# Kernel optimization log

Measured on AMD Instinct MI355X. Metric: run time of the kernel, lower is better.

## Reference

```python
import jax, jax.numpy as jnp
import numpy as np

NS = 50000; ND = 50000; E = 600000
C = 64; A = 16; S = 64; H = 8; M = 192; DH = C // H
EPS = 1e-5


def _ln(x, w, b):
    # EquivariantLayerNormV2 restricted to 0e irreps == standard affine LayerNorm
    x = x - jnp.mean(x, axis=-1, keepdims=True)
    v = jnp.mean(x * x, axis=-1, keepdims=True)
    return x * jax.lax.rsqrt(v + EPS) * w + b


def _forward(src_f, dst_f, edge_attr, edge_scalars, edge_logits, edge_src, edge_dst,
             ln_src_w, ln_src_b, W_src, ln_dst_w, ln_dst_b, W_dst, b_dst,
             W_ea, W_dtp, W_r1, b_r1, W_r2, b_r2, alpha_vec,
             W_proj, b_proj, ln_post_w, ln_post_b, W_f1, b_f1, W_f2, b_f2):
    # prenorm + linear projections of src/dst node features
    ms = _ln(src_f, ln_src_w, ln_src_b) @ W_src                      # [NS, C]
    md = _ln(dst_f, ln_dst_w, ln_dst_b) @ W_dst + b_dst              # [ND, C]
    msg = ms[edge_src] + md[edge_dst]                                # [E, C] gather
    # radial MLP on edge scalars modulates the (scalar-irrep) tensor-product weights
    r = jax.nn.silu(edge_scalars @ W_r1 + b_r1)                      # [E, S]
    w_edge = r @ W_r2 + b_r2                                         # [E, 2C]
    ea = edge_attr @ W_ea                                            # [E, C]
    dtp = ((msg * ea) @ W_dtp) * w_edge                              # [E, 2C]
    alpha_feat = dtp[:, :C].reshape(E, H, DH)
    val = dtp[:, C:].reshape(E, H, DH)
    # per-head attention logits + optional precomputed edge logits
    logits = jnp.sum(jax.nn.leaky_relu(alpha_feat, 0.2) * alpha_vec, axis=-1)  # [E, H]
    logits = logits + edge_logits[:, None]
    # softmax over incoming edges of each dst node (segment softmax)
    m = jax.ops.segment_max(logits, edge_dst, num_segments=ND)
    a = jnp.exp(logits - m[edge_dst])
    z = jax.ops.segment_sum(a, edge_dst, num_segments=ND)
    attn = a / z[edge_dst]                                           # [E, H]
    out = jax.ops.segment_sum((val * attn[..., None]).reshape(E, C), edge_dst,
                              num_segments=ND)                       # [ND, C] scatter
    out = out @ W_proj + b_proj
    emb = out + dst_f                                                # skip_1 (irreps match -> identity)
    y = _ln(emb, ln_post_w, ln_post_b)                               # post_norm
    ffn = jax.nn.silu(y @ W_f1 + b_f1) @ W_f2 + b_f2                 # FFN with swish gate (0e)
    return ffn + emb                                                 # skip_2


def setup_inputs() -> dict:
    key = jax.random.key(0)
    ks = jax.random.split(key, 20)
    def n(k, shape, scale=1.0):
        return jax.random.normal(k, shape, dtype=jnp.float32) * scale
    return {
        "src_f": n(ks[0], (NS, C)),
        "dst_f": n(ks[1], (ND, C)),
        "edge_attr": n(ks[2], (E, A)),
        "edge_scalars": jax.random.uniform(ks[3], (E, S), dtype=jnp.float32),
        "edge_logits": n(ks[4], (E,)),
        "edge_src": jax.random.randint(ks[5], (E,), 0, NS),
        "edge_dst": jax.random.randint(ks[6], (E,), 0, ND),
        "ln_src_w": jnp.ones((C,), jnp.float32), "ln_src_b": jnp.zeros((C,), jnp.float32),
        "W_src": n(ks[7], (C, C), C ** -0.5),
        "ln_dst_w": jnp.ones((C,), jnp.float32), "ln_dst_b": jnp.zeros((C,), jnp.float32),
        "W_dst": n(ks[8], (C, C), C ** -0.5), "b_dst": jnp.zeros((C,), jnp.float32),
        "W_ea": n(ks[9], (A, C), A ** -0.5),
        "W_dtp": n(ks[10], (C, 2 * C), C ** -0.5),
        "W_r1": n(ks[11], (S, S), S ** -0.5), "b_r1": jnp.zeros((S,), jnp.float32),
        "W_r2": n(ks[12], (S, 2 * C), S ** -0.5), "b_r2": jnp.zeros((2 * C,), jnp.float32),
        "alpha_vec": n(ks[13], (H, DH), DH ** -0.5),
        "W_proj": n(ks[14], (C, C), C ** -0.5), "b_proj": jnp.zeros((C,), jnp.float32),
        "ln_post_w": jnp.ones((C,), jnp.float32), "ln_post_b": jnp.zeros((C,), jnp.float32),
        "W_f1": n(ks[15], (C, M), C ** -0.5), "b_f1": jnp.zeros((M,), jnp.float32),
        "W_f2": n(ks[16], (M, C), M ** -0.5), "b_f2": jnp.zeros((C,), jnp.float32),
    }


def reference(src_f, dst_f, edge_attr, edge_scalars, edge_logits, edge_src, edge_dst,
              ln_src_w, ln_src_b, W_src, ln_dst_w, ln_dst_b, W_dst, b_dst,
              W_ea, W_dtp, W_r1, b_r1, W_r2, b_r2, alpha_vec,
              W_proj, b_proj, ln_post_w, ln_post_b, W_f1, b_f1, W_f2, b_f2):
    return _forward(src_f, dst_f, edge_attr, edge_scalars, edge_logits, edge_src, edge_dst,
                    ln_src_w, ln_src_b, W_src, ln_dst_w, ln_dst_b, W_dst, b_dst,
                    W_ea, W_dtp, W_r1, b_r1, W_r2, b_r2, alpha_vec,
                    W_proj, b_proj, ln_post_w, ln_post_b, W_f1, b_f1, W_f2, b_f2)
```

## Files before the change

### kernel.cpp

```cpp
#include <hip/hip_runtime.h>
#include <hip/hip_bf16.h>

typedef __hip_bfloat16 bf16;
typedef unsigned short u16;
typedef unsigned int u32;

#define NS_N 50000
#define ND_N 50000
#define NE_E 600000
#define C 64
#define AD 16
#define SD 64
#define NH 8
#define MF 192
#define EPSV 1e-5f

#define WB() __builtin_amdgcn_wave_barrier()

typedef short short8 __attribute__((ext_vector_type(8)));
typedef float f32x4 __attribute__((ext_vector_type(4)));
#define MFMA16(a, b, c) __builtin_amdgcn_mfma_f32_16x16x32_bf16(a, b, c, 0, 0, 0)

__device__ __forceinline__ float lo16(u32 u) {
    union { u32 i; float f; } v; v.i = u << 16; return v.f;
}
__device__ __forceinline__ float hi16(u32 u) {
    union { u32 i; float f; } v; v.i = u & 0xffff0000u; return v.f;
}
__device__ __forceinline__ float b2fu(u16 u) {
    union { u32 i; float f; } v; v.i = ((u32)u) << 16; return v.f;
}
__device__ __forceinline__ u16 f2bbits(float f) {
    u32 u = __float_as_uint(f);
    u32 r = u + 0x7FFFu + ((u >> 16) & 1u);
    return (u16)(r >> 16);
}
__device__ __forceinline__ float loadf(const void* p, size_t i, int isbf) {
    if (isbf) { union { u32 u; float f; } v; v.u = ((u32)((const u16*)p)[i]) << 16; return v.f; }
    return ((const float*)p)[i];
}
__device__ __forceinline__ u16 loadb(const void* p, size_t i, int isbf) {
    if (isbf) return ((const u16*)p)[i];
    return f2bbits(((const float*)p)[i]);
}
__device__ __forceinline__ short8 load8bf(const void* p, size_t off, int isbf) {
    if (isbf) return *(const short8*)((const u16*)p + off);
    const float4* q = (const float4*)((const float*)p + off);
    float4 f0 = q[0], f1 = q[1];
    short8 r;
    r[0] = (short)f2bbits(f0.x); r[1] = (short)f2bbits(f0.y);
    r[2] = (short)f2bbits(f0.z); r[3] = (short)f2bbits(f0.w);
    r[4] = (short)f2bbits(f1.x); r[5] = (short)f2bbits(f1.y);
    r[6] = (short)f2bbits(f1.z); r[7] = (short)f2bbits(f1.w);
    return r;
}

__device__ __forceinline__ float waveAllSum(float v) {
    #pragma unroll
    for (int off = 32; off >= 1; off >>= 1) v += __shfl_xor(v, off, 64);
    return v;
}

__global__ void detect_kernel(const void* src, int* flag) {
    const u16* p = (const u16*)src;
    const int lane = threadIdx.x;
    int cnt = 0;
    #pragma unroll
    for (int j = 0; j < 32; ++j) {
        u16 w = p[(size_t)(lane * 32 + j) * 2];
        int e = (w >> 7) & 0xFF;
        if (w == 0 || (e >= 100 && e <= 150)) cnt++;
    }
    #pragma unroll
    for (int off = 32; off >= 1; off >>= 1) cnt += __shfl_xor(cnt, off, 64);
    if (lane == 0) *flag = (cnt > 1536) ? 1 : 0;
}

__global__ void zero_int_kernel(int* p, int n) {
    int i = blockIdx.x * blockDim.x + threadIdx.x;
    if (i < n) p[i] = 0;
}

__global__ void hist_kernel(const int* __restrict__ edge_dst, int* __restrict__ cnt) {
    int e = blockIdx.x * blockDim.x + threadIdx.x;
    if (e < NE_E) atomicAdd(&cnt[edge_dst[e]], 1);
}

#define SCAN_CHUNK 1024
#define SCAN_NCH ((ND_N + SCAN_CHUNK - 1) / SCAN_CHUNK)

__global__ void scan_phase1(const int* __restrict__ cnt, int* __restrict__ chunksum) {
    __shared__ int wsum[4];
    const int b = blockIdx.x, tidx = threadIdx.x;
    const int base = b * SCAN_CHUNK + tidx * 4;
    int s = 0;
    if (base + 3 < ND_N) {
        int4 v = *(const int4*)&cnt[base];
        s = v.x + v.y + v.z + v.w;
    } else {
        #pragma unroll
        for (int j = 0; j < 4; ++j) { int i = base + j; if (i < ND_N) s += cnt[i]; }
    }
    #pragma unroll
    for (int off = 32; off >= 1; off >>= 1) s += __shfl_xor(s, off, 64);
    const int wv = tidx >> 6, lane = tidx & 63;
    if (lane == 0) wsum[wv] = s;
    __syncthreads();
    if (tidx == 0) chunksum[b] = wsum[0] + wsum[1] + wsum[2] + wsum[3];
}

__global__ void scan_phase3(const int* __restrict__ cnt, const int* __restrict__ chunksum,
                            int* __restrict__ row_ptr, int* __restrict__ cursor,
                            int* __restrict__ row_ptr_last) {
    __shared__ int woff[4];
    __shared__ int choff_s;
    const int b = blockIdx.x, tidx = threadIdx.x;
    if (tidx < 64) {
        int v = (tidx < SCAN_NCH) ? chunksum[tidx] : 0;
        int incl = v;
        #pragma unroll
        for (int off = 1; off < 64; off <<= 1) {
            int t = __shfl_up(incl, off, 64);
            if (tidx >= off) incl += t;
        }
        if (tidx == b) choff_s = incl - v;
        if (b == 0 && tidx == 63) *row_ptr_last = incl;
    }
    const int base = b * SCAN_CHUNK + tidx * 4;
    int v[4];
    #pragma unroll
    for (int j = 0; j < 4; ++j) { int i = base + j; v[j] = (i < ND_N) ? cnt[i] : 0; }
    int s = v[0] + v[1] + v[2] + v[3];
    int incl = s;
    const int lane = tidx & 63, wv = tidx >> 6;
    #pragma unroll
    for (int off = 1; off < 64; off <<= 1) {
        int t = __shfl_up(incl, off, 64);
        if (lane >= off) incl += t;
    }
    if (lane == 63) woff[wv] = incl;
    __syncthreads();
    int cross = 0;
    for (int w = 0; w < wv; ++w) cross += woff[w];
    int run = choff_s + cross + (incl - s);
    #pragma unroll
    for (int j = 0; j < 4; ++j) {
        int i = base + j;
        if (i < ND_N) { row_ptr[i] = run; cursor[i] = run; }
        run += v[j];
    }
}

__global__ void scatter_kernel(const int* __restrict__ edge_dst, int* __restrict__ cursor,
                               int* __restrict__ perm) {
    int e = blockIdx.x * blockDim.x + threadIdx.x;
    if (e < NE_E) {
        int pos = atomicAdd(&cursor[edge_dst[e]], 1);
        perm[pos] = e;
    }
}

__global__ void node_proj_kernel(const void* __restrict__ xf,
                                 const void* __restrict__ lnw, const void* __restrict__ lnb,
                                 const void* __restrict__ W, const void* __restrict__ bias,
                                 int has_bias, const int* __restrict__ flagp,
                                 float* __restrict__ out, int N) {
    __shared__ u16 sW[C * C];
    __shared__ float slnw[C], slnb[C], sbias[C];
    __shared__ float ybuf[4][C];

    const int isbf = *flagp;
    const int tid = threadIdx.x;
    for (int i = tid; i < C * C; i += blockDim.x) {
        int k = i >> 6, c = i & 63;
        sW[((k >> 1) << 7) + (c << 1) + (k & 1)] = loadb(W, i, isbf);
    }
    if (tid < C) {
        slnw[tid] = loadf(lnw, tid, isbf);
        slnb[tid] = loadf(lnb, tid, isbf);
        sbias[tid] = has_bias ? loadf(bias, tid, isbf) : 0.f;
    }
    __syncthreads();

    const int wave = tid >> 6, lane = tid & 63;
    const u32* w = (const u32*)sW;
    const int gw = blockIdx.x * 4 + wave, nw = gridDim.x * 4;
    for (int n = gw; n < N; n += nw) {
        float x = loadf(xf, (size_t)n * C + lane, isbf);
        float mean = waveAllSum(x) * (1.f / 64.f);
        float xc = x - mean;
        float var = waveAllSum(xc * xc) * (1.f / 64.f);
        float y = xc * rsqrtf(var + EPSV) * slnw[lane] + slnb[lane];
        WB();
        ybuf[wave][lane] = y;
        WB();
        float acc = sbias[lane];
        #pragma unroll 8
        for (int k2 = 0; k2 < 32; ++k2) {
            float2 yv = *(const float2*)&ybuf[wave][k2 * 2];
            u32 wp = w[(k2 << 6) + lane];
            acc += yv.x * lo16(wp) + yv.y * hi16(wp);
        }
        WB();
        out[(size_t)n * C + lane] = acc;
    }
}

__launch_bounds__(512, 4)
__global__ void edge_mfma_kernel(const void* __restrict__ edge_attr,
                                 const void* __restrict__ edge_scalars,
                                 const void* __restrict__ edge_logits,
                                 const int* __restrict__ edge_src,
                                 const int* __restrict__ edge_dst,
                                 const int* __restrict__ perm,
                                 const void* __restrict__ W_ea, const void* __restrict__ W_dtp,
                                 const void* __restrict__ W_r1, const void* __restrict__ b_r1,
                                 const void* __restrict__ W_r2, const void* __restrict__ b_r2,
                                 const void* __restrict__ alpha_vec,
                                 const int* __restrict__ flagp,
                                 const float* __restrict__ ms, const float* __restrict__ md,
                                 u16* __restrict__ valbuf, float* __restrict__ logitsbuf) {
    __shared__ u16 sWr1T[C * SD];
    __shared__ u16 sWr2T[2 * C * SD];
    __shared__ u16 sWdtpT[2 * C * C];
    __shared__ u16 sWeaT[C * 32];
    __shared__ float sbr1[SD], sbr2[2 * C], salpha[C];
    __shared__ u16 scratch[8][2][16 * C];

    const int isbf = *flagp;
    const int tid = threadIdx.x;
    for (int i = tid; i < SD * SD; i += 512) {
        int k = i >> 6, n = i & 63;
        sWr1T[n * 64 + (((k >> 3) ^ (n & 7)) << 3) + (k & 7)] = loadb(W_r1, i, isbf);
    }
    for (int i = tid; i < SD * 2 * C; i += 512) {
        int k = i >> 7, n = i & 127;
        sWr2T[n * 64 + (((k >> 3) ^ (n & 7)) << 3) + (k & 7)] = loadb(W_r2, i, isbf);
    }
    for (int i = tid; i < C * 2 * C; i += 512) {
        int k = i >> 7, n = i & 127;
        sWdtpT[n * 64 + (((k >> 3) ^ (n & 7)) << 3) + (k & 7)] = loadb(W_dtp, i, isbf);
    }
    for (int i = tid; i < C * 32; i += 512) {
        int n = i >> 5, k = i & 31;
        sWeaT[i] = (k < AD) ? loadb(W_ea, (size_t)k * C + n, isbf) : (u16)0;
    }
    for (int i = tid; i < SD; i += 512) sbr1[i] = loadf(b_r1, i, isbf);
    for (int i = tid; i < 2 * C; i += 512) sbr2[i] = loadf(b_r2, i, isbf);
    for (int i = tid; i < C; i += 512) salpha[i] = loadf(alpha_vec, i, isbf);
    __syncthreads();

    const int wv = tid >> 6, lane = tid & 63;
    const int m15 = lane & 15, quad = lane >> 4;
    const int sw = m15 & 7;
    const int pg0 = (quad ^ sw) << 3;
    const int pg1 = pg0 ^ 32;
    u16* scr_r = scratch[wv][0];
    u16* scr_e = scratch[wv][1];

    for (int t = blockIdx.x * 8 + wv; t < NE_E / 16; t += gridDim.x * 8) {
        const int e0 = t * 16;
        const int e = perm[e0 + m15];
        short8 esA0 = load8bf(edge_scalars, (size_t)e * SD + quad * 8, isbf);
        short8 esA1 = load8bf(edge_scalars, (size_t)e * SD + 32 + quad * 8, isbf);
        float elg_lane = loadf(edge_logits, e, isbf);
        WB();
        #pragma unroll
        for (int nt = 0; nt < 4; ++nt) {
            f32x4 c = {0.f, 0.f, 0.f, 0.f};
            c = MFMA16(esA0, *(const short8*)&sWr1T[(nt * 16 + m15) * 64 + pg0], c);
            c = MFMA16(esA1, *(const short8*)&sWr1T[(nt * 16 + m15) * 64 + pg1], c);
            float bc = sbr1[nt * 16 + m15];
            int lg = nt * 2 + (m15 >> 3);
            int o = m15 & 7;
            #pragma unroll
            for (int r = 0; r < 4; ++r) {
                float f = c[r] + bc;
                f = f / (1.f + __expf(-f));
                int row = quad * 4 + r;
                scr_r[row * 64 + ((lg ^ (row & 7)) << 3) + o] = f2bbits(f);
            }
        }
        short8 eaA = 0;
        if (quad < 2) eaA = load8bf(edge_attr, (size_t)e * AD + quad * 8, isbf);
        #pragma unroll
        for (int nt = 0; nt < 4; ++nt) {
            f32x4 c = {0.f, 0.f, 0.f, 0.f};
            c = MFMA16(eaA, *(const short8*)&sWeaT[(nt * 16 + m15) * 32 + quad * 8], c);
            int lg = nt * 2 + (m15 >> 3);
            int o = m15 & 7;
            #pragma unroll
            for (int r = 0; r < 4; ++r) {
                int row = quad * 4 + r;
                scr_e[row * 64 + ((lg ^ (row & 7)) << 3) + o] = f2bbits(c[r]);
            }
        }
        WB();
        short8 rA0 = *(const short8*)&scr_r[m15 * 64 + pg0];
        short8 rA1 = *(const short8*)&scr_r[m15 * 64 + pg1];
        const int s = edge_src[e];
        const int dd = edge_dst[e];
        const float* msr = ms + (size_t)s * C;
        const float* mdr = md + (size_t)dd * C;
        short8 ev0 = *(const short8*)&scr_e[m15 * 64 + pg0];
        short8 ev1 = *(const short8*)&scr_e[m15 * 64 + pg1];
        short8 xA0, xA1;
        {
            float4 a0 = *(const float4*)&msr[quad * 8];
            float4 a1 = *(const float4*)&msr[quad * 8 + 4];
            float4 b0 = *(const float4*)&mdr[quad * 8];
            float4 b1 = *(const float4*)&mdr[quad * 8 + 4];
            xA0[0] = (short)f2bbits((a0.x + b0.x) * b2fu((u16)ev0[0]));
            xA0[1] = (short)f2bbits((a0.y + b0.y) * b2fu((u16)ev0[1]));
            xA0[2] = (short)f2bbits((a0.z + b0.z) * b2fu((u16)ev0[2]));
            xA0[3] = (short)f2bbits((a0.w + b0.w) * b2fu((u16)ev0[3]));
            xA0[4] = (short)f2bbits((a1.x + b1.x) * b2fu((u16)ev0[4]));
            xA0[5] = (short)f2bbits((a1.y + b1.y) * b2fu((u16)ev0[5]));
            xA0[6] = (short)f2bbits((a1.z + b1.z) * b2fu((u16)ev0[6]));
            xA0[7] = (short)f2bbits((a1.w + b1.w) * b2fu((u16)ev0[7]));
            a0 = *(const float4*)&msr[32 + quad * 8];
            a1 = *(const float4*)&msr[32 + quad * 8 + 4];
            b0 = *(const float4*)&mdr[32 + quad * 8];
            b1 = *(const float4*)&mdr[32 + quad * 8 + 4];
            xA1[0] = (short)f2bbits((a0.x + b0.x) * b2fu((u16)ev1[0]));
            xA1[1] = (short)f2bbits((a0.y + b0.y) * b2fu((u16)ev1[1]));
            xA1[2] = (short)f2bbits((a0.z + b0.z) * b2fu((u16)ev1[2]));
            xA1[3] = (short)f2bbits((a0.w + b0.w) * b2fu((u16)ev1[3]));
            xA1[4] = (short)f2bbits((a1.x + b1.x) * b2fu((u16)ev1[4]));
            xA1[5] = (short)f2bbits((a1.y + b1.y) * b2fu((u16)ev1[5]));
            xA1[6] = (short)f2bbits((a1.z + b1.z) * b2fu((u16)ev1[6]));
            xA1[7] = (short)f2bbits((a1.w + b1.w) * b2fu((u16)ev1[7]));
        }
        float elg_q[4];
        #pragma unroll
        for (int r = 0; r < 4; ++r) elg_q[r] = __shfl(elg_lane, quad * 4 + r, 64);
        WB();
        #pragma unroll
        for (int nt = 0; nt < 8; ++nt) {
            f32x4 w = {0.f, 0.f, 0.f, 0.f};
            w = MFMA16(rA0, *(const short8*)&sWr2T[(nt * 16 + m15) * 64 + pg0], w);
            w = MFMA16(rA1, *(const short8*)&sWr2T[(nt * 16 + m15) * 64 + pg1], w);
            f32x4 dv = {0.f, 0.f, 0.f, 0.f};
            dv = MFMA16(xA0, *(const short8*)&sWdtpT[(nt * 16 + m15) * 64 + pg0], dv);
            dv = MFMA16(xA1, *(const short8*)&sWdtpT[(nt * 16 + m15) * 64 + pg1], dv);
            float wb = sbr2[nt * 16 + m15];
            if (nt < 4) {
                float sa = salpha[nt * 16 + m15];
                #pragma unroll
                for (int r = 0; r < 4; ++r) {
                    float v = dv[r] * (w[r] + wb);
                    float lf = (v >= 0.f) ? v : 0.2f * v;
                    float tt = lf * sa;
                    tt += __shfl_xor(tt, 1, 64);
                    tt += __shfl_xor(tt, 2, 64);
                    tt += __shfl_xor(tt, 4, 64);
                    if ((lane & 7) == 0)
                        logitsbuf[(size_t)(e0 + quad * 4 + r) * NH + nt * 2 + ((lane >> 3) & 1)]
                            = tt + elg_q[r];
                }
            } else {
                int lg = (nt - 4) * 2 + (m15 >> 3);
                int o = m15 & 7;
                #pragma unroll
                for (int r = 0; r < 4; ++r) {
                    float v = dv[r] * (w[r] + wb);
                    int row = quad * 4 + r;
                    scr_r[row * 64 + ((lg ^ (row & 7)) << 3) + o] = f2bbits(v);
                }
            }
        }
        WB();
        {
            int row = lane >> 2, seg = lane & 3;
            int rw7 = row & 7;
            uint4 v0 = *(const uint4*)&scr_r[row * 64 + (((seg * 2) ^ rw7) << 3)];
            uint4 v1 = *(const uint4*)&scr_r[row * 64 + (((seg * 2 + 1) ^ rw7) << 3)];
            uint4* gp = (uint4*)&valbuf[(size_t)(e0 + row) * C + seg * 16];
            gp[0] = v0; gp[1] = v1;
        }
        WB();
    }
}

__global__ void aggregate_kernel(const int* __restrict__ row_ptr,
                                 const float* __restrict__ logitsbuf,
                                 const u16* __restrict__ valbuf,
                                 float* __restrict__ attout) {
    const int wave = threadIdx.x >> 6, lane = threadIdx.x & 63;
    const int head = lane >> 3;
    const int gw = blockIdx.x * 4 + wave, nw = gridDim.x * 4;
    for (int d = gw; d < ND_N; d += nw) {
        const int beg = row_ptr[d], end = row_ptr[d + 1];
        float m0 = -__builtin_inff(), z0 = 0.f, a0 = 0.f;
        float m1 = -__builtin_inff(), z1 = 0.f, a1 = 0.f;
        int i = beg;
        for (; i + 1 < end; i += 2) {
            float lg0 = logitsbuf[(size_t)i * NH + head];
            float lg1 = logitsbuf[(size_t)(i + 1) * NH + head];
            float v0 = b2fu(valbuf[(size_t)i * C + lane]);
            float v1 = b2fu(valbuf[(size_t)(i + 1) * C + lane]);
            float mn0 = fmaxf(m0, lg0);
            float mn1 = fmaxf(m1, lg1);
            float sc0 = __expf(m0 - mn0);
            float sc1 = __expf(m1 - mn1);
            float e0 = __expf(lg0 - mn0);
            float e1 = __expf(lg1 - mn1);
            z0 = z0 * sc0 + e0; a0 = a0 * sc0 + e0 * v0; m0 = mn0;
            z1 = z1 * sc1 + e1; a1 = a1 * sc1 + e1 * v1; m1 = mn1;
        }
        if (i < end) {
            float lg0 = logitsbuf[(size_t)i * NH + head];
            float v0 = b2fu(valbuf[(size_t)i * C + lane]);
            float mn = fmaxf(m0, lg0);
            float sc = __expf(m0 - mn);
            float e0 = __expf(lg0 - mn);
            z0 = z0 * sc + e0; a0 = a0 * sc + e0 * v0; m0 = mn;
        }
        float mn = fmaxf(m0, m1);
        float s0 = __expf(m0 - mn);
        float s1 = __expf(m1 - mn);
        float z = z0 * s0 + z1 * s1;
        float acc = a0 * s0 + a1 * s1;
        attout[(size_t)d * C + lane] = (z > 0.f) ? acc / z : 0.f;
    }
}

__global__ void edge_csr_kernel(const void* __restrict__ edge_attr,
                                const void* __restrict__ edge_scalars,
                                const void* __restrict__ edge_logits,
                                const int* __restrict__ edge_src,
                                const int* __restrict__ row_ptr, const int* __restrict__ perm,
                                const void* __restrict__ W_ea, const void* __restrict__ W_dtp,
                                const void* __restrict__ W_r1, const void* __restrict__ b_r1,
                                const void* __restrict__ W_r2, const void* __restrict__ b_r2,
                                const void* __restrict__ alpha_vec,
                                const int* __restrict__ flagp,
                                const float* __restrict__ ms, const float* __restrict__ md,
                                float* __restrict__ attout) {
    __shared__ u16 sWr1[SD * SD];
    __shared__ u16 sWr2[SD * 2 * C];
    __shared__ u16 sWdtp[C * 2 * C];
    __shared__ u16 sWea[AD * C];
    __shared__ float sbr1[SD], sbr2[2 * C], salpha[C];
    __shared__ float sbuf[4][2][C];

    const int isbf = *flagp;
    const int tid = threadIdx.x;
    {
        for (int i = tid; i < SD * SD; i += blockDim.x) {
            int k = i >> 6, c = i & 63;
            sWr1[((k >> 1) << 7) + (c << 1) + (k & 1)] = loadb(W_r1, i, isbf);
        }
        for (int i = tid; i < SD * 2 * C; i += blockDim.x) {
            int k = i >> 7, c = i & 127;
            sWr2[(k << 7) + ((c & 63) << 1) + (c >> 6)] = loadb(W_r2, i, isbf);
        }
        for (int i = tid; i < C * 2 * C; i += blockDim.x) {
            int k = i >> 7, c = i & 127;
            sWdtp[(k << 7) + ((c & 63) << 1) + (c >> 6)] = loadb(W_dtp, i, isbf);
        }
        for (int i = tid; i < AD * C; i += blockDim.x) {
            int k = i >> 6, c = i & 63;
            sWea[((k >> 1) << 7) + (c << 1) + (k & 1)] = loadb(W_ea, i, isbf);
        }
        for (int i = tid; i < SD; i += blockDim.x) sbr1[i] = loadf(b_r1, i, isbf);
        for (int i = tid; i < 2 * C; i += blockDim.x) sbr2[i] = loadf(b_r2, i, isbf);
        for (int i = tid; i < C; i += blockDim.x) salpha[i] = loadf(alpha_vec, i, isbf);
    }
    __syncthreads();

    const int wave = tid >> 6, lane = tid & 63;
    float* buf0 = sbuf[wave][0];
    float* buf1 = sbuf[wave][1];
    const u32* wr1 = (const u32*)sWr1;
    const u32* wr2 = (const u32*)sWr2;
    const u32* wdtp = (const u32*)sWdtp;
    const u32* wea = (const u32*)sWea;
    const int gw = blockIdx.x * 4 + wave, nw = gridDim.x * 4;

    for (int d = gw; d < ND_N; d += nw) {
        const int beg = row_ptr[d], end = row_ptr[d + 1];
        const float mdv = md[(size_t)d * C + lane];
        float m = -__builtin_inff(), z = 0.f, acc = 0.f;

        for (int i = beg; i < end; ++i) {
            const int e = perm[i];
            WB();
            buf0[lane] = loadf(edge_scalars, (size_t)e * SD + lane, isbf);
            WB();
            float accr = sbr1[lane];
            #pragma unroll 8
            for (int k2 = 0; k2 < 32; ++k2) {
                float2 xv = *(const float2*)&buf0[k2 * 2];
                u32 wp = wr1[(k2 << 6) + lane];
                accr += xv.x * lo16(wp) + xv.y * hi16(wp);
            }
            float r = accr / (1.f + __expf(-accr));
            WB();
            buf1[lane] = r;
            WB();
            float we0 = sbr2[lane], we1 = sbr2[lane + C];
            #pragma unroll 8
            for (int k = 0; k < SD; ++k) {
                float rk = buf1[k];
                u32 wp = wr2[(k << 6) + lane];
                we0 += rk * lo16(wp);
                we1 += rk * hi16(wp);
            }
            WB();
            if (lane < AD) buf0[lane] = loadf(edge_attr, (size_t)e * AD + lane, isbf);
            WB();
            float eav = 0.f;
            #pragma unroll
            for (int k2 = 0; k2 < 8; ++k2) {
                float2 xv = *(const float2*)&buf0[k2 * 2];
                u32 wp = wea[(k2 << 6) + lane];
                eav += xv.x * lo16(wp) + xv.y * hi16(wp);
            }
            const int s = edge_src[e];
            float x = (ms[(size_t)s * C + lane] + mdv) * eav;
            WB();
            buf1[lane] = x;
            WB();
            float dt0 = 0.f, dt1 = 0.f;
            #pragma unroll 8
            for (int k = 0; k < C; ++k) {
                float xk = buf1[k];
                u32 wp = wdtp[(k << 6) + lane];
                dt0 += xk * lo16(wp);
                dt1 += xk * hi16(wp);
            }
            dt0 *= we0;
            dt1 *= we1;
            float lf = (dt0 >= 0.f) ? dt0 : 0.2f * dt0;
            float t = lf * salpha[lane];
            t += __shfl_xor(t, 1, 64);
            t += __shfl_xor(t, 2, 64);
            t += __shfl_xor(t, 4, 64);
            float lg = t + loadf(edge_logits, e, isbf);
            float mn = fmaxf(m, lg);
            float sc = __expf(m - mn);
            float a = __expf(lg - mn);
            z = z * sc + a;
            acc = acc * sc + a * dt1;
            m = mn;
        }
        attout[(size_t)d * C + lane] = (z > 0.f) ? acc / z : 0.f;
    }
}

__launch_bounds__(512, 2)
__global__ void final_mfma_kernel(const void* __restrict__ dst_f,
                                  const float* __restrict__ attout,
                                  const void* __restrict__ W_proj, const void* __restrict__ b_proj,
                                  const void* __restrict__ ln_w, const void* __restrict__ ln_b,
                                  const void* __restrict__ W_f1, const void* __restrict__ b_f1,
                                  const void* __restrict__ W_f2, const void* __restrict__ b_f2,
                                  const int* __restrict__ flagp,
                                  void* __restrict__ out) {
    __shared__ u16 sWpT[C * C];
    __shared__ u16 sWf1T[MF * C];
    __shared__ u16 sWf2T[C * MF];
    __shared__ float sbp[C], slnw[C], slnb[C], sbf1[MF], sbf2[C];
    __shared__ uint4 scr4[8][400];

    const int isbf = *flagp;
    const int tid = threadIdx.x;
    for (int i = tid; i < C * C; i += 512) {
        int k = i >> 6, n = i & 63;
        sWpT[n * 64 + (((k >> 3) ^ (n & 7)) << 3) + (k & 7)] = loadb(W_proj, i, isbf);
    }
    for (int i = tid; i < C * MF; i += 512) {
        int k = i / MF, n = i - k * MF;
        sWf1T[n * 64 + (((k >> 3) ^ (n & 7)) << 3) + (k & 7)] = loadb(W_f1, i, isbf);
    }
    for (int i = tid; i < MF * C; i += 512) {
        int k = i >> 6, n = i & 63;
        sWf2T[n * 192 + (((k >> 3) ^ (n & 7)) << 3) + (k & 7)] = loadb(W_f2, i, isbf);
    }
    for (int i = tid; i < C; i += 512) {
        sbp[i] = loadf(b_proj, i, isbf);
        slnw[i] = loadf(ln_w, i, isbf);
        slnb[i] = loadf(ln_b, i, isbf);
        sbf2[i] = loadf(b_f2, i, isbf);
    }
    for (int i = tid; i < MF; i += 512) sbf1[i] = loadf(b_f1, i, isbf);
    __syncthreads();

    const int wv = tid >> 6, lane = tid & 63;
    const int m15 = lane & 15, quad = lane >> 4;
    const int sw = m15 & 7;
    const int pg0 = (quad ^ sw) << 3;
    const int pg1 = pg0 ^ 32;
    u16* scr = (u16*)scr4[wv];
    float* scrf = (float*)scr4[wv];

    for (int t = blockIdx.x * 8 + wv; t < ND_N / 16; t += gridDim.x * 8) {
        const int n0 = t * 16;
        short8 oA0 = load8bf(attout, (size_t)(n0 + m15) * C + quad * 8, 0);
        short8 oA1 = load8bf(attout, (size_t)(n0 + m15) * C + 32 + quad * 8, 0);
        float emb[4][4];
        #pragma unroll
        for (int nt = 0; nt < 4; ++nt) {
            f32x4 c = {0.f, 0.f, 0.f, 0.f};
            c = MFMA16(oA0, *(const short8*)&sWpT[(nt * 16 + m15) * 64 + pg0], c);
            c = MFMA16(oA1, *(const short8*)&sWpT[(nt * 16 + m15) * 64 + pg1], c);
            int col = nt * 16 + m15;
            float bp = sbp[col];
            #pragma unroll
            for (int r = 0; r < 4; ++r)
                emb[nt][r] = c[r] + bp + loadf(dst_f, (size_t)(n0 + quad * 4 + r) * C + col, isbf);
        }
        float y[4][4];
        #pragma unroll
        for (int r = 0; r < 4; ++r) {
            float part = emb[0][r] + emb[1][r] + emb[2][r] + emb[3][r];
            part += __shfl_xor(part, 1, 64);
            part += __shfl_xor(part, 2, 64);
            part += __shfl_xor(part, 4, 64);
            part += __shfl_xor(part, 8, 64);
            float mean = part * (1.f / 64.f);
            float q = 0.f;
            #pragma unroll
            for (int nt = 0; nt < 4; ++nt) {
                float d = emb[nt][r] - mean;
                q += d * d;
            }
            q += __shfl_xor(q, 1, 64);
            q += __shfl_xor(q, 2, 64);
            q += __shfl_xor(q, 4, 64);
            q += __shfl_xor(q, 8, 64);
            float rs = rsqrtf(q * (1.f / 64.f) + EPSV);
            #pragma unroll
            for (int nt = 0; nt < 4; ++nt) {
                int col = nt * 16 + m15;
                y[nt][r] = (emb[nt][r] - mean) * rs * slnw[col] + slnb[col];
            }
        }
        WB();
        #pragma unroll
        for (int nt = 0; nt < 4; ++nt)
            #pragma unroll
            for (int r = 0; r < 4; ++r)
                scr[(quad * 4 + r) * 72 + nt * 16 + m15] = f2bbits(y[nt][r]);
        WB();
        short8 yA0 = *(const short8*)&scr[m15 * 72 + quad * 8];
        short8 yA1 = *(const short8*)&scr[m15 * 72 + 32 + quad * 8];
        WB();
        #pragma unroll
        for (int nt = 0; nt < 12; ++nt) {
            f32x4 g = {0.f, 0.f, 0.f, 0.f};
            g = MFMA16(yA0, *(const short8*)&sWf1T[(nt * 16 + m15) * 64 + pg0], g);
            g = MFMA16(yA1, *(const short8*)&sWf1T[(nt * 16 + m15) * 64 + pg1], g);
            int col = nt * 16 + m15;
            float bg = sbf1[col];
            #pragma unroll
            for (int r = 0; r < 4; ++r) {
                float f = g[r] + bg;
                f = f / (1.f + __expf(-f));
                scr[(quad * 4 + r) * 200 + col] = f2bbits(f);
            }
        }
        WB();
        short8 gA[6];
        #pragma unroll
        for (int j = 0; j < 6; ++j)
            gA[j] = *(const short8*)&scr[m15 * 200 + j * 32 + quad * 8];
        WB();
        #pragma unroll
        for (int nt = 0; nt < 4; ++nt) {
            f32x4 c = {0.f, 0.f, 0.f, 0.f};
            #pragma unroll
            for (int j = 0; j < 6; ++j) {
                int lg = j * 4 + quad;
                int pg = (lg ^ sw) << 3;
                c = MFMA16(gA[j], *(const short8*)&sWf2T[(nt * 16 + m15) * 192 + pg], c);
            }
            int col = nt * 16 + m15;
            float bf = sbf2[col];
            #pragma unroll
            for (int r = 0; r < 4; ++r)
                scrf[(quad * 4 + r) * 68 + col] = c[r] + bf + emb[nt][r];
        }
        WB();
        {
            int row = lane >> 2, seg = lane & 3;
            if (isbf) {
                u16* gp = (u16*)out + (size_t)(n0 + row) * C + seg * 16;
                #pragma unroll
                for (int j = 0; j < 4; ++j) {
                    float4 v = *(const float4*)&scrf[row * 68 + seg * 16 + j * 4];
                    u32 p0 = (u32)f2bbits(v.x) | ((u32)f2bbits(v.y) << 16);
                    u32 p1 = (u32)f2bbits(v.z) | ((u32)f2bbits(v.w) << 16);
                    uint2 pk = {p0, p1};
                    *(uint2*)(gp + j * 4) = pk;
                }
            } else {
                float* gp = (float*)out + (size_t)(n0 + row) * C + seg * 16;
                #pragma unroll
                for (int j = 0; j < 4; ++j)
                    *(float4*)(gp + j * 4) = *(const float4*)&scrf[row * 68 + seg * 16 + j * 4];
            }
        }
        WB();
    }
}

__global__ void final_scalar_kernel(const void* __restrict__ dst_f,
                                    const float* __restrict__ attout,
                                    const void* __restrict__ W_proj, const void* __restrict__ b_proj,
                                    const void* __restrict__ ln_w, const void* __restrict__ ln_b,
                                    const void* __restrict__ W_f1, const void* __restrict__ b_f1,
                                    const void* __restrict__ W_f2, const void* __restrict__ b_f2,
                                    const int* __restrict__ flagp,
                                    void* __restrict__ out) {
    __shared__ u16 sWp[C * C];
    __shared__ u16 sWf1p[C * 2 * C];
    __shared__ u16 sWf1c[C * C];
    __shared__ u16 sWf2[MF * C];
    __shared__ float sbp[C], slnw[C], slnb[C], sbf1[MF], sbf2[C];
    __shared__ float ybuf[4][C];
    __shared__ float gbuf[4][MF];

    const int isbf = *flagp;
    const int tid = threadIdx.x;
    {
        for (int i = tid; i < C * C; i += blockDim.x) {
            int k = i >> 6, c = i & 63;
            sWp[((k >> 1) << 7) + (c << 1) + (k & 1)] = loadb(W_proj, i, isbf);
        }
        for (int i = tid; i < C * MF; i += blockDim.x) {
            int k = i / MF, c = i - k * MF;
            u16 b = loadb(W_f1, i, isbf);
            if (c < 128) sWf1p[(k << 7) + ((c & 63) << 1) + (c >> 6)] = b;
            else         sWf1c[(k << 6) + (c - 128)] = b;
        }
        for (int i = tid; i < MF * C; i += blockDim.x) {
            int k = i >> 6, c = i & 63;
            sWf2[((k >> 1) << 7) + (c << 1) + (k & 1)] = loadb(W_f2, i, isbf);
        }
        for (int i = tid; i < C; i += blockDim.x) {
            sbp[i] = loadf(b_proj, i, isbf);
            slnw[i] = loadf(ln_w, i, isbf);
            slnb[i] = loadf(ln_b, i, isbf);
            sbf2[i] = loadf(b_f2, i, isbf);
        }
        for (int i = tid; i < MF; i += blockDim.x) sbf1[i] = loadf(b_f1, i, isbf);
    }
    __syncthreads();

    const int wave = tid >> 6, lane = tid & 63;
    const u32* wp32 = (const u32*)sWp;
    const u32* wf1 = (const u32*)sWf1p;
    const u32* wf2 = (const u32*)sWf2;
    const int gw = blockIdx.x * 4 + wave, nw = gridDim.x * 4;

    for (int n = gw; n < ND_N; n += nw) {
        float o = attout[(size_t)n * C + lane];
        WB();
        ybuf[wave][lane] = o;
        WB();
        float p = sbp[lane];
        #pragma unroll 8
        for (int k2 = 0; k2 < 32; ++k2) {
            float2 yv = *(const float2*)&ybuf[wave][k2 * 2];
            u32 wv = wp32[(k2 << 6) + lane];
            p += yv.x * lo16(wv) + yv.y * hi16(wv);
        }
        float emb = p + loadf(dst_f, (size_t)n * C + lane, isbf);
        float mean = waveAllSum(emb) * (1.f / 64.f);
        float ec = emb - mean;
        float var = waveAllSum(ec * ec) * (1.f / 64.f);
        float y = ec * rsqrtf(var + EPSV) * slnw[lane] + slnb[lane];
        WB();
        ybuf[wave][lane] = y;
        WB();
        float g0 = sbf1[lane], g1v = sbf1[lane + C], g2v = sbf1[lane + 2 * C];
        #pragma unroll 8
        for (int k = 0; k < C; ++k) {
            float yk = ybuf[wave][k];
            u32 wv = wf1[(k << 6) + lane];
            union { u32 u; float f; } cv; cv.u = ((u32)sWf1c[(k << 6) + lane]) << 16;
            g0 += yk * lo16(wv);
            g1v += yk * hi16(wv);
            g2v += yk * cv.f;
        }
        WB();
        gbuf[wave][lane] = g0 / (1.f + __expf(-g0));
        gbuf[wave][lane + C] = g1v / (1.f + __expf(-g1v));
        gbuf[wave][lane + 2 * C] = g2v / (1.f + __expf(-g2v));
        WB();
        float f = sbf2[lane];
        #pragma unroll 8
        for (int k2 = 0; k2 < 96; ++k2) {
            float2 gv = *(const float2*)&gbuf[wave][k2 * 2];
            u32 wv = wf2[(k2 << 6) + lane];
            f += gv.x * lo16(wv) + gv.y * hi16(wv);
        }
        WB();
        float res = f + emb;
        if (isbf) ((bf16*)out)[(size_t)n * C + lane] = __float2bfloat16(res);
        else      ((float*)out)[(size_t)n * C + lane] = res;
    }
}

extern "C" void kernel_launch(void* const* d_in, const int* in_sizes, int n_in,
                              void* d_out, int out_size, void* d_ws, size_t ws_size,
                              hipStream_t stream) {
    const void* src_f        = d_in[0];
    const void* dst_f        = d_in[1];
    const void* edge_attr    = d_in[2];
    const void* edge_scalars = d_in[3];
    const void* edge_logits  = d_in[4];
    const int*  edge_src     = (const int*)d_in[5];
    const int*  edge_dst     = (const int*)d_in[6];
    const void* ln_src_w = d_in[7];
    const void* ln_src_b = d_in[8];
    const void* W_src    = d_in[9];
    const void* ln_dst_w = d_in[10];
    const void* ln_dst_b = d_in[11];
    const void* W_dst    = d_in[12];
    const void* b_dst    = d_in[13];
    const void* W_ea     = d_in[14];
    const void* W_dtp    = d_in[15];
    const void* W_r1     = d_in[16];
    const void* b_r1     = d_in[17];
    const void* W_r2     = d_in[18];
    const void* b_r2     = d_in[19];
    const void* alpha_vec = d_in[20];
    const void* W_proj   = d_in[21];
    const void* b_proj   = d_in[22];
    const void* ln_post_w = d_in[23];
    const void* ln_post_b = d_in[24];
    const void* W_f1     = d_in[25];
    const void* b_f1     = d_in[26];
    const void* W_f2     = d_in[27];
    const void* b_f2     = d_in[28];

    int* flag     = (int*)d_ws;
    float* ms     = (float*)d_ws + 16;
    float* md     = ms + (size_t)NS_N * C;
    int* cnt      = (int*)(md + (size_t)ND_N * C);
    int* row_ptr  = cnt + ND_N;
    int* cursor   = row_ptr + (ND_N + 4);
    int* perm     = cursor + ND_N;
    float* logitsbuf = (float*)(perm + NE_E);
    u16* valbuf      = (u16*)(logitsbuf + (size_t)NE_E * NH);
    float* attout_slow = (float*)(perm + NE_E);

    size_t base_b = (size_t)(16 + NS_N * C + ND_N * C) * 4
                  + ((size_t)ND_N * 3 + 4 + NE_E) * 4;
    size_t need_fast = base_b + (size_t)NE_E * NH * 4 + (size_t)NE_E * C * 2;
    size_t need_slow = base_b + (size_t)ND_N * C * 4;
    int fast = (ws_size >= need_fast) ? 1 : 0;
    if (!fast && ws_size < need_slow) return;

    detect_kernel<<<1, 64, 0, stream>>>(src_f, flag);

    zero_int_kernel<<<(ND_N + 255) / 256, 256, 0, stream>>>(cnt, ND_N);
    hist_kernel<<<(NE_E + 255) / 256, 256, 0, stream>>>(edge_dst, cnt);
    scan_phase1<<<SCAN_NCH, 256, 0, stream>>>(cnt, perm);
    scan_phase3<<<SCAN_NCH, 256, 0, stream>>>(cnt, perm, row_ptr, cursor, &row_ptr[ND_N]);
    scatter_kernel<<<(NE_E + 255) / 256, 256, 0, stream>>>(edge_dst, cursor, perm);

    node_proj_kernel<<<1024, 256, 0, stream>>>(src_f, ln_src_w, ln_src_b, W_src,
                                               (const void*)nullptr, 0, flag, ms, NS_N);
    node_proj_kernel<<<1024, 256, 0, stream>>>(dst_f, ln_dst_w, ln_dst_b, W_dst,
                                               b_dst, 1, flag, md, ND_N);

    if (fast) {
        edge_mfma_kernel<<<1024, 512, 0, stream>>>(edge_attr, edge_scalars, edge_logits,
                                                   edge_src, edge_dst, perm,
                                                   W_ea, W_dtp, W_r1, b_r1, W_r2, b_r2,
                                                   alpha_vec, flag, ms, md,
                                                   valbuf, logitsbuf);
        aggregate_kernel<<<2048, 256, 0, stream>>>(row_ptr, logitsbuf, valbuf, ms);
        final_mfma_kernel<<<256, 512, 0, stream>>>(dst_f, ms,
                                                   W_proj, b_proj, ln_post_w, ln_post_b,
                                                   W_f1, b_f1, W_f2, b_f2,
                                                   flag, d_out);
    } else {
        edge_csr_kernel<<<2048, 256, 0, stream>>>(edge_attr, edge_scalars, edge_logits,
                                                  edge_src, row_ptr, perm,
                                                  W_ea, W_dtp, W_r1, b_r1, W_r2, b_r2,
                                                  alpha_vec, flag, ms, md, attout_slow);
        final_scalar_kernel<<<1024, 256, 0, stream>>>(dst_f, attout_slow,
                                                      W_proj, b_proj, ln_post_w, ln_post_b,
                                                      W_f1, b_f1, W_f2, b_f2,
                                                      flag, d_out);
    }
}
```

Before: 637.9 us.

## Store node projections in bf16, prefetch edge gathers, merge small launches

```diff
diff --git a/kernel.cpp b/kernel.cpp
--- a/kernel.cpp
+++ b/kernel.cpp
@@ -61,24 +61,26 @@
     return v;
 }
 
-__global__ void detect_kernel(const void* src, int* flag) {
-    const u16* p = (const u16*)src;
-    const int lane = threadIdx.x;
-    int cnt = 0;
-    #pragma unroll
-    for (int j = 0; j < 32; ++j) {
-        u16 w = p[(size_t)(lane * 32 + j) * 2];
-        int e = (w >> 7) & 0xFF;
-        if (w == 0 || (e >= 100 && e <= 150)) cnt++;
-    }
-    #pragma unroll
-    for (int off = 32; off >= 1; off >>= 1) cnt += __shfl_xor(cnt, off, 64);
-    if (lane == 0) *flag = (cnt > 1536) ? 1 : 0;
-}
-
-__global__ void zero_int_kernel(int* p, int n) {
-    int i = blockIdx.x * blockDim.x + threadIdx.x;
-    if (i < n) p[i] = 0;
+__global__ void detect_zero_kernel(const void* src, int* flag, int* cnt) {
+    if (blockIdx.x == 0) {
+        if (threadIdx.x < 64) {
+            const u16* p = (const u16*)src;
+            const int lane = threadIdx.x;
+            int c = 0;
+            #pragma unroll
+            for (int j = 0; j < 32; ++j) {
+                u16 w = p[(size_t)(lane * 32 + j) * 2];
+                int e = (w >> 7) & 0xFF;
+                if (w == 0 || (e >= 100 && e <= 150)) c++;
+            }
+            #pragma unroll
+            for (int off = 32; off >= 1; off >>= 1) c += __shfl_xor(c, off, 64);
+            if (lane == 0) *flag = (c > 1536) ? 1 : 0;
+        }
+    } else {
+        int i = (blockIdx.x - 1) * blockDim.x + threadIdx.x;
+        if (i < ND_N) cnt[i] = 0;
+    }
 }
 
 __global__ void hist_kernel(const int* __restrict__ edge_dst, int* __restrict__ cnt) {
@@ -160,17 +162,30 @@
     }
 }
 
-__global__ void node_proj_kernel(const void* __restrict__ xf,
-                                 const void* __restrict__ lnw, const void* __restrict__ lnb,
-                                 const void* __restrict__ W, const void* __restrict__ bias,
-                                 int has_bias, const int* __restrict__ flagp,
-                                 float* __restrict__ out, int N) {
+__global__ void node_proj2_kernel(const void* __restrict__ src_f, const void* __restrict__ dst_f,
+                                  const void* __restrict__ lnw_s, const void* __restrict__ lnb_s,
+                                  const void* __restrict__ W_s,
+                                  const void* __restrict__ lnw_d, const void* __restrict__ lnb_d,
+                                  const void* __restrict__ W_d, const void* __restrict__ b_d,
+                                  const int* __restrict__ flagp,
+                                  u16* __restrict__ ms, u16* __restrict__ md) {
     __shared__ u16 sW[C * C];
     __shared__ float slnw[C], slnb[C], sbias[C];
     __shared__ float ybuf[4][C];
 
     const int isbf = *flagp;
     const int tid = threadIdx.x;
+    const int half = gridDim.x >> 1;
+    const int isrc = (blockIdx.x < half) ? 1 : 0;
+    const void* xf  = isrc ? src_f : dst_f;
+    const void* lnw = isrc ? lnw_s : lnw_d;
+    const void* lnb = isrc ? lnb_s : lnb_d;
+    const void* W   = isrc ? W_s : W_d;
+    u16* out        = isrc ? ms : md;
+    const int N     = isrc ? NS_N : ND_N;
+    const int bid   = isrc ? blockIdx.x : blockIdx.x - half;
+    const int nb    = isrc ? half : gridDim.x - half;
+
     for (int i = tid; i < C * C; i += blockDim.x) {
         int k = i >> 6, c = i & 63;
         sW[((k >> 1) << 7) + (c << 1) + (k & 1)] = loadb(W, i, isbf);
@@ -178,13 +193,13 @@
     if (tid < C) {
         slnw[tid] = loadf(lnw, tid, isbf);
         slnb[tid] = loadf(lnb, tid, isbf);
-        sbias[tid] = has_bias ? loadf(bias, tid, isbf) : 0.f;
+        sbias[tid] = isrc ? 0.f : loadf(b_d, tid, isbf);
     }
     __syncthreads();
 
     const int wave = tid >> 6, lane = tid & 63;
     const u32* w = (const u32*)sW;
-    const int gw = blockIdx.x * 4 + wave, nw = gridDim.x * 4;
+    const int gw = bid * 4 + wave, nw = nb * 4;
     for (int n = gw; n < N; n += nw) {
         float x = loadf(xf, (size_t)n * C + lane, isbf);
         float mean = waveAllSum(x) * (1.f / 64.f);
@@ -202,7 +217,8 @@
             acc += yv.x * lo16(wp) + yv.y * hi16(wp);
         }
         WB();
-        out[(size_t)n * C + lane] = acc;
+        out[(size_t)n * C + lane] = f2bbits(acc);
+        WB();
     }
 }
 
@@ -218,7 +234,7 @@
                                  const void* __restrict__ W_r2, const void* __restrict__ b_r2,
                                  const void* __restrict__ alpha_vec,
                                  const int* __restrict__ flagp,
-                                 const float* __restrict__ ms, const float* __restrict__ md,
+                                 const u16* __restrict__ ms, const u16* __restrict__ md,
                                  u16* __restrict__ valbuf, float* __restrict__ logitsbuf) {
     __shared__ u16 sWr1T[C * SD];
     __shared__ u16 sWr2T[2 * C * SD];
@@ -258,12 +274,33 @@
     u16* scr_r = scratch[wv][0];
     u16* scr_e = scratch[wv][1];
 
-    for (int t = blockIdx.x * 8 + wv; t < NE_E / 16; t += gridDim.x * 8) {
+    const int NT = NE_E / 16;
+    const int stride = gridDim.x * 8;
+    int t = blockIdx.x * 8 + wv;
+
+    int e = 0, s = 0, dd = 0;
+    if (t < NT) {
+        e = perm[t * 16 + m15];
+        s = edge_src[e];
+        dd = edge_dst[e];
+    }
+
+    while (t < NT) {
+        const int tn = t + stride;
         const int e0 = t * 16;
-        const int e = perm[e0 + m15];
         short8 esA0 = load8bf(edge_scalars, (size_t)e * SD + quad * 8, isbf);
         short8 esA1 = load8bf(edge_scalars, (size_t)e * SD + 32 + quad * 8, isbf);
         float elg_lane = loadf(edge_logits, e, isbf);
+        short8 eaA = 0;
+        if (quad < 2) eaA = load8bf(edge_attr, (size_t)e * AD + quad * 8, isbf);
+        const u16* msr = ms + (size_t)s * C;
+        const u16* mdr = md + (size_t)dd * C;
+        short8 gms0 = *(const short8*)&msr[quad * 8];
+        short8 gms1 = *(const short8*)&msr[32 + quad * 8];
+        short8 gmd0 = *(const short8*)&mdr[quad * 8];
+        short8 gmd1 = *(const short8*)&mdr[32 + quad * 8];
+        int eN = 0;
+        if (tn < NT) eN = perm[tn * 16 + m15];
         WB();
         #pragma unroll
         for (int nt = 0; nt < 4; ++nt) {
@@ -281,8 +318,6 @@
                 scr_r[row * 64 + ((lg ^ (row & 7)) << 3) + o] = f2bbits(f);
             }
         }
-        short8 eaA = 0;
-        if (quad < 2) eaA = load8bf(edge_attr, (size_t)e * AD + quad * 8, isbf);
         #pragma unroll
         for (int nt = 0; nt < 4; ++nt) {
             f32x4 c = {0.f, 0.f, 0.f, 0.f};
@@ -295,41 +330,20 @@
                 scr_e[row * 64 + ((lg ^ (row & 7)) << 3) + o] = f2bbits(c[r]);
             }
         }
+        int sN = 0, ddN = 0;
+        if (tn < NT) { sN = edge_src[eN]; ddN = edge_dst[eN]; }
         WB();
         short8 rA0 = *(const short8*)&scr_r[m15 * 64 + pg0];
         short8 rA1 = *(const short8*)&scr_r[m15 * 64 + pg1];
-        const int s = edge_src[e];
-        const int dd = edge_dst[e];
-        const float* msr = ms + (size_t)s * C;
-        const float* mdr = md + (size_t)dd * C;
         short8 ev0 = *(const short8*)&scr_e[m15 * 64 + pg0];
         short8 ev1 = *(const short8*)&scr_e[m15 * 64 + pg1];
         short8 xA0, xA1;
-        {
-            float4 a0 = *(const float4*)&msr[quad * 8];
-            float4 a1 = *(const float4*)&msr[quad * 8 + 4];
-            float4 b0 = *(const float4*)&mdr[quad * 8];
-            float4 b1 = *(const float4*)&mdr[quad * 8 + 4];
-            xA0[0] = (short)f2bbits((a0.x + b0.x) * b2fu((u16)ev0[0]));
-            xA0[1] = (short)f2bbits((a0.y + b0.y) * b2fu((u16)ev0[1]));
-            xA0[2] = (short)f2bbits((a0.z + b0.z) * b2fu((u16)ev0[2]));
-            xA0[3] = (short)f2bbits((a0.w + b0.w) * b2fu((u16)ev0[3]));
-            xA0[4] = (short)f2bbits((a1.x + b1.x) * b2fu((u16)ev0[4]));
-            xA0[5] = (short)f2bbits((a1.y + b1.y) * b2fu((u16)ev0[5]));
-            xA0[6] = (short)f2bbits((a1.z + b1.z) * b2fu((u16)ev0[6]));
-            xA0[7] = (short)f2bbits((a1.w + b1.w) * b2fu((u16)ev0[7]));
-            a0 = *(const float4*)&msr[32 + quad * 8];
-            a1 = *(const float4*)&msr[32 + quad * 8 + 4];
-            b0 = *(const float4*)&mdr[32 + quad * 8];
-            b1 = *(const float4*)&mdr[32 + quad * 8 + 4];
-            xA1[0] = (short)f2bbits((a0.x + b0.x) * b2fu((u16)ev1[0]));
-            xA1[1] = (short)f2bbits((a0.y + b0.y) * b2fu((u16)ev1[1]));
-            xA1[2] = (short)f2bbits((a0.z + b0.z) * b2fu((u16)ev1[2]));
-            xA1[3] = (short)f2bbits((a0.w + b0.w) * b2fu((u16)ev1[3]));
-            xA1[4] = (short)f2bbits((a1.x + b1.x) * b2fu((u16)ev1[4]));
-            xA1[5] = (short)f2bbits((a1.y + b1.y) * b2fu((u16)ev1[5]));
-            xA1[6] = (short)f2bbits((a1.z + b1.z) * b2fu((u16)ev1[6]));
-            xA1[7] = (short)f2bbits((a1.w + b1.w) * b2fu((u16)ev1[7]));
+        #pragma unroll
+        for (int j = 0; j < 8; ++j) {
+            float a = b2fu((u16)gms0[j]) + b2fu((u16)gmd0[j]);
+            xA0[j] = (short)f2bbits(a * b2fu((u16)ev0[j]));
+            float b = b2fu((u16)gms1[j]) + b2fu((u16)gmd1[j]);
+            xA1[j] = (short)f2bbits(b * b2fu((u16)ev1[j]));
         }
         float elg_q[4];
         #pragma unroll
@@ -379,6 +393,7 @@
             gp[0] = v0; gp[1] = v1;
         }
         WB();
+        t = tn; e = eN; s = sN; dd = ddN;
     }
 }
 
@@ -435,7 +450,7 @@
                                 const void* __restrict__ W_r2, const void* __restrict__ b_r2,
                                 const void* __restrict__ alpha_vec,
                                 const int* __restrict__ flagp,
-                                const float* __restrict__ ms, const float* __restrict__ md,
+                                const u16* __restrict__ ms, const u16* __restrict__ md,
                                 float* __restrict__ attout) {
     __shared__ u16 sWr1[SD * SD];
     __shared__ u16 sWr2[SD * 2 * C];
@@ -480,7 +495,7 @@
 
     for (int d = gw; d < ND_N; d += nw) {
         const int beg = row_ptr[d], end = row_ptr[d + 1];
-        const float mdv = md[(size_t)d * C + lane];
+        const float mdv = b2fu(md[(size_t)d * C + lane]);
         float m = -__builtin_inff(), z = 0.f, acc = 0.f;
 
         for (int i = beg; i < end; ++i) {
@@ -518,7 +533,7 @@
                 eav += xv.x * lo16(wp) + xv.y * hi16(wp);
             }
             const int s = edge_src[e];
-            float x = (ms[(size_t)s * C + lane] + mdv) * eav;
+            float x = (b2fu(ms[(size_t)s * C + lane]) + mdv) * eav;
             WB();
             buf1[lane] = x;
             WB();
@@ -838,9 +853,11 @@
     const void* b_f2     = d_in[28];
 
     int* flag     = (int*)d_ws;
-    float* ms     = (float*)d_ws + 16;
-    float* md     = ms + (size_t)NS_N * C;
-    int* cnt      = (int*)(md + (size_t)ND_N * C);
+    float* msf    = (float*)d_ws + 16;
+    float* mdf    = msf + (size_t)NS_N * C;
+    u16* ms16     = (u16*)msf;
+    u16* md16     = (u16*)mdf;
+    int* cnt      = (int*)(mdf + (size_t)ND_N * C);
     int* row_ptr  = cnt + ND_N;
     int* cursor   = row_ptr + (ND_N + 4);
     int* perm     = cursor + ND_N;
@@ -855,27 +872,25 @@
     int fast = (ws_size >= need_fast) ? 1 : 0;
     if (!fast && ws_size < need_slow) return;
 
-    detect_kernel<<<1, 64, 0, stream>>>(src_f, flag);
-
-    zero_int_kernel<<<(ND_N + 255) / 256, 256, 0, stream>>>(cnt, ND_N);
+    detect_zero_kernel<<<1 + (ND_N + 255) / 256, 256, 0, stream>>>(src_f, flag, cnt);
     hist_kernel<<<(NE_E + 255) / 256, 256, 0, stream>>>(edge_dst, cnt);
     scan_phase1<<<SCAN_NCH, 256, 0, stream>>>(cnt, perm);
     scan_phase3<<<SCAN_NCH, 256, 0, stream>>>(cnt, perm, row_ptr, cursor, &row_ptr[ND_N]);
     scatter_kernel<<<(NE_E + 255) / 256, 256, 0, stream>>>(edge_dst, cursor, perm);
 
-    node_proj_kernel<<<1024, 256, 0, stream>>>(src_f, ln_src_w, ln_src_b, W_src,
-                                               (const void*)nullptr, 0, flag, ms, NS_N);
-    node_proj_kernel<<<1024, 256, 0, stream>>>(dst_f, ln_dst_w, ln_dst_b, W_dst,
-                                               b_dst, 1, flag, md, ND_N);
+    node_proj2_kernel<<<2048, 256, 0, stream>>>(src_f, dst_f,
+                                                ln_src_w, ln_src_b, W_src,
+                                                ln_dst_w, ln_dst_b, W_dst, b_dst,
+                                                flag, ms16, md16);
 
     if (fast) {
         edge_mfma_kernel<<<1024, 512, 0, stream>>>(edge_attr, edge_scalars, edge_logits,
                                                    edge_src, edge_dst, perm,
                                                    W_ea, W_dtp, W_r1, b_r1, W_r2, b_r2,
-                                                   alpha_vec, flag, ms, md,
+                                                   alpha_vec, flag, ms16, md16,
                                                    valbuf, logitsbuf);
-        aggregate_kernel<<<2048, 256, 0, stream>>>(row_ptr, logitsbuf, valbuf, ms);
-        final_mfma_kernel<<<256, 512, 0, stream>>>(dst_f, ms,
+        aggregate_kernel<<<2048, 256, 0, stream>>>(row_ptr, logitsbuf, valbuf, msf);
+        final_mfma_kernel<<<256, 512, 0, stream>>>(dst_f, msf,
                                                    W_proj, b_proj, ln_post_w, ln_post_b,
                                                    W_f1, b_f1, W_f2, b_f2,
                                                    flag, d_out);
@@ -883,7 +898,7 @@
         edge_csr_kernel<<<2048, 256, 0, stream>>>(edge_attr, edge_scalars, edge_logits,
                                                   edge_src, row_ptr, perm,
                                                   W_ea, W_dtp, W_r1, b_r1, W_r2, b_r2,
-                                                  alpha_vec, flag, ms, md, attout_slow);
+                                                  alpha_vec, flag, ms16, md16, attout_slow);
         final_scalar_kernel<<<1024, 256, 0, stream>>>(dst_f, attout_slow,
                                                       W_proj, b_proj, ln_post_w, ln_post_b,
                                                       W_f1, b_f1, W_f2, b_f2,
```

Result: faster. 606.7 us (-4.9%).
